# Kernel optimization log

Measured on AMD Instinct MI355X. Metric: run time of the kernel, lower is better.

The kernel has to match this reference:

```python
import jax, jax.numpy as jnp
import numpy as np

HEADS = 8
POINTS = 4
EPS = 1e-5


def _layernorm(x, w, b):
    m = jnp.mean(x, axis=-1, keepdims=True)
    v = jnp.var(x, axis=-1, keepdims=True)
    return (x - m) / jnp.sqrt(v + EPS) * w + b


def _msdeform_attn(x, ref, value, H, W, Wv, bv, Woff, boff, Wa, ba, Wout, bout):
    # x: (N, Lq, C) queries; value: (N, H*W, C); ref: (N, Lq, 1, 2) in [0,1]
    N, Lq, C = x.shape
    hd = C // HEADS
    # value projection, split heads -> (N, heads, HW, hd)
    v = (value @ Wv + bv).reshape(N, H * W, HEADS, hd).transpose(0, 2, 1, 3)
    # per-query learned offsets and attention weights
    off = (x @ Woff + boff).reshape(N, Lq, HEADS, POINTS, 2)
    attw = jax.nn.softmax((x @ Wa + ba).reshape(N, Lq, HEADS, POINTS), axis=-1)
    offset_normalizer = jnp.array([W, H], dtype=x.dtype)
    # sampling locations in normalized [0,1] coords: (N, Lq, heads, points, 2)
    loc = ref[:, :, None, :, :] + off / offset_normalizer
    # grid_sample bilinear, align_corners=False, zeros padding: pixel = loc*size - 0.5
    gx = loc[..., 0] * W - 0.5
    gy = loc[..., 1] * H - 0.5
    x0 = jnp.floor(gx)
    y0 = jnp.floor(gy)
    wx = gx - x0
    wy = gy - y0
    x0i = x0.astype(jnp.int32)
    y0i = y0.astype(jnp.int32)

    def gather(xi, yi):  # (N,Lq,heads,points) int -> (N,heads,Lq,points,hd), zero outside
        valid = ((xi >= 0) & (xi < W) & (yi >= 0) & (yi < H))
        idx = (jnp.clip(yi, 0, H - 1) * W + jnp.clip(xi, 0, W - 1)).transpose(0, 2, 1, 3)
        g = jnp.take_along_axis(v, idx.reshape(N, HEADS, Lq * POINTS)[..., None], axis=2)
        return g.reshape(N, HEADS, Lq, POINTS, hd) * valid.transpose(0, 2, 1, 3)[..., None].astype(v.dtype)

    def cw(w_):  # corner weight to (N,heads,Lq,points,1)
        return w_.transpose(0, 2, 1, 3)[..., None]

    samp = (gather(x0i, y0i) * cw((1 - wx) * (1 - wy))
            + gather(x0i + 1, y0i) * cw(wx * (1 - wy))
            + gather(x0i, y0i + 1) * cw((1 - wx) * wy)
            + gather(x0i + 1, y0i + 1) * cw(wx * wy))
    out = jnp.einsum('nhlpd,nlhp->nlhd', samp, attw).reshape(N, Lq, C)
    return out @ Wout + bout


def setup_inputs() -> dict:
    key = jax.random.key(0)
    ks = jax.random.split(key, 12)
    N, Lq, C, H, W = 4, 6400, 256, 80, 80
    hid = 4 * C
    hp2 = HEADS * POINTS * 2
    hp = HEADS * POINTS

    def w(k, shape, s=0.02):
        return jax.random.normal(k, shape, dtype=jnp.float32) * s

    return {
        'x': jax.random.normal(ks[0], (N, Lq, C), dtype=jnp.float32),
        'ref': jax.random.uniform(ks[1], (N, Lq, 1, 2), dtype=jnp.float32),
        'value': jax.random.normal(ks[2], (N, Lq, C), dtype=jnp.float32),
        'H': H, 'W': W,
        'ln1_w': jnp.ones((C,), jnp.float32), 'ln1_b': jnp.zeros((C,), jnp.float32),
        'ln2_w': jnp.ones((C,), jnp.float32), 'ln2_b': jnp.zeros((C,), jnp.float32),
        'Wv': w(ks[3], (C, C)), 'bv': jnp.zeros((C,), jnp.float32),
        'Woff': w(ks[4], (C, hp2), 0.01), 'boff': w(ks[5], (hp2,), 0.5),
        'Wa': w(ks[6], (C, hp)), 'ba': jnp.zeros((hp,), jnp.float32),
        'Wout': w(ks[7], (C, C)), 'bout': jnp.zeros((C,), jnp.float32),
        'W1': w(ks[8], (C, hid)), 'b1': jnp.zeros((hid,), jnp.float32),
        'W2': w(ks[9], (hid, C)), 'b2': jnp.zeros((C,), jnp.float32),
    }


def reference(x, ref, value, H, W, ln1_w, ln1_b, ln2_w, ln2_b, Wv, bv, Woff, boff, Wa, ba, Wout, bout, W1, b1, W2, b2):
    # x = x + attn(norm1(x), ref, value); LayerScale/DropPath are identity (init_values=None, drop_path=0)
    a = _msdeform_attn(_layernorm(x, ln1_w, ln1_b), ref, value, H, W, Wv, bv, Woff, boff, Wa, ba, Wout, bout)
    x = x + a
    # x = x + mlp(norm2(x))
    h = _layernorm(x, ln2_w, ln2_b)
    h = jax.nn.gelu(h @ W1 + b1, approximate=False)
    return x + (h @ W2 + b2)
```

## Files before the change

kernel.cpp:

```cpp
#include <hip/hip_runtime.h>

#define NB    4
#define LQ    6400
#define CC    256
#define HH    80
#define WW    80
#define HWSZ  (HH*WW)
#define RTOT  (NB*LQ)
#define HID   1024

typedef __attribute__((ext_vector_type(8))) short bf16x8;
typedef __attribute__((ext_vector_type(4))) float f32x4;

__device__ __forceinline__ float bf2f(unsigned short u) {
    unsigned int i = ((unsigned int)u) << 16;
    float f; __builtin_memcpy(&f, &i, 4); return f;
}
__device__ __forceinline__ unsigned short f2bf(float f) {
    unsigned int i; __builtin_memcpy(&i, &f, 4);
    unsigned int r = i + 0x7fffu + ((i >> 16) & 1u);
    return (unsigned short)(r >> 16);
}

__global__ void cvt_k(const float* __restrict__ in, unsigned short* __restrict__ out, int n4) {
    int i = blockIdx.x * 256 + threadIdx.x;
    if (i < n4) {
        float4 u = ((const float4*)in)[i];
        ushort4 o;
        o.x = f2bf(u.x); o.y = f2bf(u.y); o.z = f2bf(u.z); o.w = f2bf(u.w);
        ((ushort4*)out)[i] = o;
    }
}

__global__ void prep_k(const float* __restrict__ Wv,   const float* __restrict__ Wout,
                       const float* __restrict__ W1,   const float* __restrict__ W2,
                       const float* __restrict__ Woff, const float* __restrict__ Wa,
                       const float* __restrict__ boff, const float* __restrict__ ba,
                       unsigned short* __restrict__ wtv,  unsigned short* __restrict__ woutS,
                       unsigned short* __restrict__ w1s,  unsigned short* __restrict__ w2s,
                       unsigned short* __restrict__ woas, float* __restrict__ b_oa) {
    int idx = blockIdx.x * 256 + threadIdx.x;
    if (idx < 65536) {
        int n = idx >> 8, k = idx & 255;
        wtv[idx] = f2bf(Wv[(size_t)k * 256 + n]);
        return;
    }
    idx -= 65536;
    if (idx < 32768) {
        int n = idx & 1023, kq = idx >> 10;
        int kb = (kq >> 2) * 32 + (kq & 3) * 8;
        unsigned short* d = w1s + (size_t)idx * 8;
        #pragma unroll
        for (int j = 0; j < 8; ++j) d[j] = f2bf(W1[(size_t)(kb + j) * 1024 + n]);
        return;
    }
    idx -= 32768;
    if (idx < 32768) {
        int n = idx & 255, kq = idx >> 8;
        int kb = (kq >> 2) * 32 + (kq & 3) * 8;
        unsigned short* d = w2s + (size_t)idx * 8;
        #pragma unroll
        for (int j = 0; j < 8; ++j) d[j] = f2bf(W2[(size_t)(kb + j) * 256 + n]);
        return;
    }
    idx -= 32768;
    if (idx < 8192) {
        int n = idx & 255, kq = idx >> 8;
        int kb = (kq >> 2) * 32 + (kq & 3) * 8;
        unsigned short* d = woutS + (size_t)idx * 8;
        #pragma unroll
        for (int j = 0; j < 8; ++j) d[j] = f2bf(Wout[(size_t)(kb + j) * 256 + n]);
        return;
    }
    idx -= 8192;
    if (idx < 4096) {
        int n = idx & 127, kq = idx >> 7;
        int kb = (kq >> 2) * 32 + (kq & 3) * 8;
        unsigned short* d = woas + (size_t)idx * 8;
        #pragma unroll
        for (int j = 0; j < 8; ++j) {
            float v = 0.f;
            if (n < 64)      v = Woff[(size_t)(kb + j) * 64 + n];
            else if (n < 96) v = Wa[(size_t)(kb + j) * 32 + (n - 64)];
            d[j] = f2bf(v);
        }
        return;
    }
    idx -= 4096;
    if (idx < 96) b_oa[idx] = idx < 64 ? boff[idx] : ba[idx - 64];
}

__device__ __forceinline__ void ln_stage(const float* __restrict__ xbase,
                                         const float* __restrict__ lw,
                                         const float* __restrict__ lb,
                                         unsigned short* hblob, int t) {
    int r = t >> 3, sub = t & 7;
    const float* xr = xbase + (size_t)r * CC;
    float4 xv[4][2];
    float s = 0.f, s2 = 0.f;
    #pragma unroll
    for (int jj = 0; jj < 4; ++jj) {
        #pragma unroll
        for (int u = 0; u < 2; ++u) {
            float4 v = *(const float4*)(xr + sub * 8 + jj * 64 + u * 4);
            xv[jj][u] = v;
            s  += v.x + v.y + v.z + v.w;
            s2 += v.x*v.x + v.y*v.y + v.z*v.z + v.w*v.w;
        }
    }
    #pragma unroll
    for (int m = 1; m < 8; m <<= 1) {
        s  += __shfl_xor(s,  m);
        s2 += __shfl_xor(s2, m);
    }
    float mean = s * (1.0f / CC);
    float var  = s2 * (1.0f / CC) - mean * mean;
    float rstd = rsqrtf(fmaxf(var, 0.0f) + 1e-5f);
    #pragma unroll
    for (int jj = 0; jj < 4; ++jj) {
        int c0 = sub * 8 + jj * 64;
        float4 w0 = *(const float4*)(lw + c0);
        float4 w1 = *(const float4*)(lw + c0 + 4);
        float4 bb0 = *(const float4*)(lb + c0);
        float4 bb1 = *(const float4*)(lb + c0 + 4);
        bf16x8 o;
        o[0] = (short)f2bf((xv[jj][0].x - mean) * rstd * w0.x + bb0.x);
        o[1] = (short)f2bf((xv[jj][0].y - mean) * rstd * w0.y + bb0.y);
        o[2] = (short)f2bf((xv[jj][0].z - mean) * rstd * w0.z + bb0.z);
        o[3] = (short)f2bf((xv[jj][0].w - mean) * rstd * w0.w + bb0.w);
        o[4] = (short)f2bf((xv[jj][1].x - mean) * rstd * w1.x + bb1.x);
        o[5] = (short)f2bf((xv[jj][1].y - mean) * rstd * w1.y + bb1.y);
        o[6] = (short)f2bf((xv[jj][1].z - mean) * rstd * w1.z + bb1.z);
        o[7] = (short)f2bf((xv[jj][1].w - mean) * rstd * w1.w + bb1.w);
        int kq = sub + jj * 8;
        *(bf16x8*)((char*)hblob + kq * 1040 + r * 16) = o;
    }
}

template<int EPI, bool OF32>
__global__ __launch_bounds__(256) void gemm_t(const unsigned short* __restrict__ A,
                                              const unsigned short* __restrict__ Bt,
                                              const float* __restrict__ bias,
                                              const float* __restrict__ res,
                                              void* __restrict__ Cout_,
                                              int M, int Nv, int K) {
    __shared__ unsigned short Als[64 * 32];
    __shared__ unsigned short Bls[128 * 32];
    int lane = threadIdx.x & 63;
    int wave = threadIdx.x >> 6;
    int quad = lane >> 4;
    int l16  = lane & 15;
    int m0 = blockIdx.x * 64;
    int n0 = blockIdx.y * 128;
    int wm = (wave & 1) * 32;
    int wn = (wave >> 1) * 64;

    f32x4 acc[2][4];
    #pragma unroll
    for (int i = 0; i < 2; ++i)
        #pragma unroll
        for (int j = 0; j < 4; ++j)
            acc[i][j] = (f32x4){0.f, 0.f, 0.f, 0.f};

    int srow = lane >> 2;
    int scol = (lane & 3) * 8;
    const unsigned short* Ag = A  + (size_t)(m0 + wave * 16 + srow) * K + scol;
    const unsigned short* Bg = Bt + (size_t)(n0 + wave * 32 + srow) * K + scol;
    unsigned short* Alp = &Als[wave * 512];
    unsigned short* Blp = &Bls[wave * 1024];

    for (int k0 = 0; k0 < K; k0 += 32) {
        __syncthreads();
        __builtin_amdgcn_global_load_lds(
            (const __attribute__((address_space(1))) void*)(Ag + k0),
            (__attribute__((address_space(3))) void*)Alp, 16, 0, 0);
        #pragma unroll
        for (int t = 0; t < 2; ++t) {
            __builtin_amdgcn_global_load_lds(
                (const __attribute__((address_space(1))) void*)(Bg + (size_t)t * 16 * K + k0),
                (__attribute__((address_space(3))) void*)(Blp + t * 512), 16, 0, 0);
        }
        __builtin_amdgcn_s_waitcnt(0);
        __syncthreads();

        bf16x8 af[2], bfr[4];
        #pragma unroll
        for (int i = 0; i < 2; ++i)
            af[i] = *(const bf16x8*)&Als[(wm + i * 16 + l16) * 32 + quad * 8];
        #pragma unroll
        for (int j = 0; j < 4; ++j)
            bfr[j] = *(const bf16x8*)&Bls[(wn + j * 16 + l16) * 32 + quad * 8];
        #pragma unroll
        for (int i = 0; i < 2; ++i)
            #pragma unroll
            for (int j = 0; j < 4; ++j)
                acc[i][j] = __builtin_amdgcn_mfma_f32_16x16x32_bf16(af[i], bfr[j], acc[i][j], 0, 0, 0);
    }

    #pragma unroll
    for (int j = 0; j < 4; ++j) {
        int cbase = n0 + wn + j * 16;
        if (cbase >= Nv) continue;
        int col = cbase + l16;
        float bv = bias[col];
        #pragma unroll
        for (int i = 0; i < 2; ++i) {
            #pragma unroll
            for (int r = 0; r < 4; ++r) {
                int row = m0 + wm + i * 16 + quad * 4 + r;
                float val = acc[i][j][r] + bv;
                if (EPI == 2) val += res[(size_t)row * Nv + col];
                if (OF32) ((float*)Cout_)[(size_t)row * Nv + col] = val;
                else      ((unsigned short*)Cout_)[(size_t)row * Nv + col] = f2bf(val);
            }
        }
    }
}

__global__ __launch_bounds__(512) void lnoa_k(
        const float* __restrict__ x, const float* __restrict__ lw, const float* __restrict__ lb,
        const unsigned short* __restrict__ woas, const float* __restrict__ b_oa,
        unsigned short* __restrict__ oa) {
    __shared__ char lds_raw[33280];
    unsigned short* hblob = (unsigned short*)lds_raw;
    int t = threadIdx.x;
    int lane = t & 63, wave = t >> 6;
    int quad = lane >> 4, l16 = lane & 15;
    int row0 = blockIdx.x * 64;

    ln_stage(x + (size_t)row0 * CC, lw, lb, hblob, t);
    __syncthreads();

    if (wave < 6) {
        f32x4 acc[4];
        #pragma unroll
        for (int qt = 0; qt < 4; ++qt) acc[qt] = (f32x4){0.f, 0.f, 0.f, 0.f};
        #pragma unroll
        for (int kb = 0; kb < 8; ++kb) {
            bf16x8 a1 = *(const bf16x8*)(woas + ((size_t)(kb * 4 + quad) * 128 + wave * 16 + l16) * 8);
            #pragma unroll
            for (int qt = 0; qt < 4; ++qt) {
                bf16x8 bf = *(const bf16x8*)((char*)hblob + (kb * 4 + quad) * 1040 + (qt * 16 + l16) * 16);
                acc[qt] = __builtin_amdgcn_mfma_f32_16x16x32_bf16(a1, bf, acc[qt], 0, 0, 0);
            }
        }
        int n0 = wave * 16 + quad * 4;
        float4 bb = *(const float4*)(b_oa + n0);
        const float* bp = (const float*)&bb;
        #pragma unroll
        for (int qt = 0; qt < 4; ++qt) {
            unsigned long long pk = 0;
            #pragma unroll
            for (int r = 0; r < 4; ++r)
                pk |= ((unsigned long long)f2bf(acc[qt][r] + bp[r])) << (16 * r);
            *(unsigned long long*)(oa + (size_t)(row0 + qt * 16 + l16) * 96 + n0) = pk;
        }
    }
}

__global__ __launch_bounds__(512) void samwout_k(
        const unsigned short* __restrict__ v,
        const float* __restrict__ ref,
        const unsigned short* __restrict__ oa,
        const unsigned short* __restrict__ woutS,
        const float* __restrict__ bout,
        const float* __restrict__ x,
        float* __restrict__ x2) {
    __shared__ char lds_raw[57856];
    unsigned short* hblob = (unsigned short*)lds_raw;
    short4* sidx = (short4*)(lds_raw + 33280);
    float4* sw   = (float4*)(lds_raw + 41472);
    float* trans = (float*)lds_raw;

    int t = threadIdx.x;
    int lane = t & 63, wave = t >> 6;
    int quad = lane >> 4, l16 = lane & 15;
    int row0 = blockIdx.x * 64;
    int nb = blockIdx.x / (LQ / 64);

    for (int half = 0; half < 2; ++half) {
        int rbase = half * 32;
        #pragma unroll
        for (int s = 0; s < 2; ++s) {
            int e = t + s * 512;
            int q = e >> 5, sub = e & 31, h = sub >> 2, p = sub & 3;
            int row = row0 + rbase + q;
            float refx = ref[row * 2 + 0];
            float refy = ref[row * 2 + 1];
            const unsigned short* oar = oa + (size_t)row * 96;
            float ox = bf2f(oar[(h * 4 + p) * 2 + 0]);
            float oy = bf2f(oar[(h * 4 + p) * 2 + 1]);
            float l  = bf2f(oar[64 + h * 4 + p]);
            float m = fmaxf(l, __shfl_xor(l, 1));
            m = fmaxf(m, __shfl_xor(m, 2));
            float ee = __expf(l - m);
            float ss = ee + __shfl_xor(ee, 1);
            ss = ss + __shfl_xor(ss, 2);
            float wp = ee / ss;

            float gx = (refx + ox * (1.0f / WW)) * WW - 0.5f;
            float gy = (refy + oy * (1.0f / HH)) * HH - 0.5f;
            float fx = floorf(gx), fy = floorf(gy);
            float wx = gx - fx, wy = gy - fy;
            int x0 = (int)fx, y0 = (int)fy;
            int x1 = x0 + 1, y1 = y0 + 1;
            bool vx0 = (unsigned)x0 < WW, vx1 = (unsigned)x1 < WW;
            bool vy0 = (unsigned)y0 < HH, vy1 = (unsigned)y1 < HH;
            float w00 = (vx0 && vy0) ? wp * (1.f - wx) * (1.f - wy) : 0.f;
            float w10 = (vx1 && vy0) ? wp * wx * (1.f - wy)         : 0.f;
            float w01 = (vx0 && vy1) ? wp * (1.f - wx) * wy         : 0.f;
            float w11 = (vx1 && vy1) ? wp * wx * wy                 : 0.f;
            int cx0 = min(max(x0, 0), WW - 1), cx1 = min(max(x1, 0), WW - 1);
            int cy0 = min(max(y0, 0), HH - 1), cy1 = min(max(y1, 0), HH - 1);
            sidx[e] = (short4){(short)(cy0 * WW + cx0), (short)(cy0 * WW + cx1),
                               (short)(cy1 * WW + cx0), (short)(cy1 * WW + cx1)};
            sw[e]   = (float4){w00, w10, w01, w11};
        }
        __syncthreads();
        #pragma unroll
        for (int s = 0; s < 2; ++s) {
            int c = t + s * 512;
            int q = c >> 5, sub = c & 31, h = sub >> 2, cg = sub & 3;
            const unsigned short* base = v + (size_t)nb * HWSZ * CC + h * 32 + cg * 8;
            float acc[8];
            #pragma unroll
            for (int j = 0; j < 8; ++j) acc[j] = 0.f;
            #pragma unroll
            for (int p = 0; p < 4; ++p) {
                int e = q * 32 + h * 4 + p;
                short4 I = sidx[e];
                float4 Wt = sw[e];
                const short* Ip = (const short*)&I;
                const float* Wp = (const float*)&Wt;
                #pragma unroll
                for (int cn = 0; cn < 4; ++cn) {
                    bf16x8 u = *(const bf16x8*)(base + (size_t)(unsigned short)Ip[cn] * CC);
                    float wgt = Wp[cn];
                    #pragma unroll
                    for (int j = 0; j < 8; ++j)
                        acc[j] += wgt * bf2f((unsigned short)u[j]);
                }
            }
            bf16x8 o;
            #pragma unroll
            for (int j = 0; j < 8; ++j) o[j] = (short)f2bf(acc[j]);
            *(bf16x8*)((char*)hblob + sub * 1040 + (rbase + q) * 16) = o;
        }
        __syncthreads();
    }

    f32x4 acc2[2][4];
    #pragma unroll
    for (int a = 0; a < 2; ++a)
        #pragma unroll
        for (int b = 0; b < 4; ++b)
            acc2[a][b] = (f32x4){0.f, 0.f, 0.f, 0.f};
    #pragma unroll
    for (int kb = 0; kb < 8; ++kb) {
        bf16x8 a2[2], bf[4];
        #pragma unroll
        for (int ct = 0; ct < 2; ++ct)
            a2[ct] = *(const bf16x8*)(woutS + ((size_t)(kb * 4 + quad) * 256 + wave * 32 + ct * 16 + l16) * 8);
        #pragma unroll
        for (int qt = 0; qt < 4; ++qt)
            bf[qt] = *(const bf16x8*)((char*)hblob + (kb * 4 + quad) * 1040 + (qt * 16 + l16) * 16);
        #pragma unroll
        for (int ct = 0; ct < 2; ++ct)
            #pragma unroll
            for (int qt = 0; qt < 4; ++qt)
                acc2[ct][qt] = __builtin_amdgcn_mfma_f32_16x16x32_bf16(a2[ct], bf[qt], acc2[ct][qt], 0, 0, 0);
    }

    for (int p = 0; p < 2; ++p) {
        __syncthreads();
        #pragma unroll
        for (int qi = 0; qi < 2; ++qi) {
            int qt = p * 2 + qi;
            int qlocal = qt * 16 + l16 - p * 32;
            #pragma unroll
            for (int ct = 0; ct < 2; ++ct) {
                int c4 = wave * 8 + ct * 4 + quad;
                *(f32x4*)(trans + qlocal * 260 + c4 * 4) = acc2[ct][qt];
            }
        }
        __syncthreads();
        int rr = t >> 4;
        int c4b = t & 15;
        int row = row0 + p * 32 + rr;
        #pragma unroll
        for (int i = 0; i < 4; ++i) {
            int c4 = i * 16 + c4b;
            f32x4 vv = *(const f32x4*)(trans + rr * 260 + c4 * 4);
            int c = c4 * 4;
            float4 xv = *(const float4*)(x + (size_t)row * CC + c);
            float4 bb = *(const float4*)(bout + c);
            float4 o;
            o.x = vv[0] + xv.x + bb.x;
            o.y = vv[1] + xv.y + bb.y;
            o.z = vv[2] + xv.z + bb.z;
            o.w = vv[3] + xv.w + bb.w;
            *(float4*)(x2 + (size_t)row * CC + c) = o;
        }
    }
}

__global__ __launch_bounds__(512) void mlp_k(
        const float* __restrict__ x2,
        const float* __restrict__ lw,
        const float* __restrict__ lb,
        const unsigned short* __restrict__ w1s,
        const float* __restrict__ b1,
        const unsigned short* __restrict__ w2s,
        const float* __restrict__ b2,
        float* __restrict__ out) {
    __shared__ char lds_raw[66560];
    unsigned short* hblob = (unsigned short*)lds_raw;
    unsigned short* h1b0  = (unsigned short*)(lds_raw + 33280);
    unsigned short* h1b1  = (unsigned short*)(lds_raw + 49920);
    float* trans = (float*)lds_raw;

    int t = threadIdx.x;
    int lane = t & 63, wave = t >> 6;
    int quad = lane >> 4, l16 = lane & 15;
    int row0 = blockIdx.x * 64;

    ln_stage(x2 + (size_t)row0 * CC, lw, lb, hblob, t);
    __syncthreads();

    f32x4 acc2[2][4];
    #pragma unroll
    for (int a = 0; a < 2; ++a)
        #pragma unroll
        for (int b = 0; b < 4; ++b)
            acc2[a][b] = (f32x4){0.f, 0.f, 0.f, 0.f};

    auto s1 = [&](int hc, unsigned short* dst) {
        f32x4 a[4];
        #pragma unroll
        for (int qt = 0; qt < 4; ++qt) a[qt] = (f32x4){0.f, 0.f, 0.f, 0.f};
        #pragma unroll
        for (int kb = 0; kb < 8; ++kb) {
            bf16x8 a1 = *(const bf16x8*)(w1s + ((size_t)(kb * 4 + quad) * 1024 + hc * 128 + wave * 16 + l16) * 8);
            #pragma unroll
            for (int qt = 0; qt < 4; ++qt) {
                bf16x8 bf = *(const bf16x8*)((char*)hblob + (kb * 4 + quad) * 1040 + (qt * 16 + l16) * 16);
                a[qt] = __builtin_amdgcn_mfma_f32_16x16x32_bf16(a1, bf, a[qt], 0, 0, 0);
            }
        }
        int hl = wave * 16 + quad * 4;
        float4 bb = *(const float4*)(b1 + hc * 128 + hl);
        const float* bp = (const float*)&bb;
        #pragma unroll
        for (int qt = 0; qt < 4; ++qt) {
            unsigned long long pk = 0;
            #pragma unroll
            for (int r = 0; r < 4; ++r) {
                float val = a[qt][r] + bp[r];
                val = 0.5f * val * (1.0f + erff(val * 0.70710678118654752f));
                pk |= ((unsigned long long)f2bf(val)) << (16 * r);
            }
            *(unsigned long long*)((char*)dst + (hl >> 3) * 1040 + (qt * 16 + l16) * 16 + (hl & 7) * 2) = pk;
        }
    };

    auto s2 = [&](int hc, const unsigned short* src) {
        #pragma unroll
        for (int k2 = 0; k2 < 4; ++k2) {
            bf16x8 a2[2], bf[4];
            #pragma unroll
            for (int ct = 0; ct < 2; ++ct)
                a2[ct] = *(const bf16x8*)(w2s + ((size_t)((hc * 4 + k2) * 4 + quad) * 256 + wave * 32 + ct * 16 + l16) * 8);
            #pragma unroll
            for (int qt = 0; qt < 4; ++qt)
                bf[qt] = *(const bf16x8*)((const char*)src + (k2 * 4 + quad) * 1040 + (qt * 16 + l16) * 16);
            #pragma unroll
            for (int ct = 0; ct < 2; ++ct)
                #pragma unroll
                for (int qt = 0; qt < 4; ++qt)
                    acc2[ct][qt] = __builtin_amdgcn_mfma_f32_16x16x32_bf16(a2[ct], bf[qt], acc2[ct][qt], 0, 0, 0);
        }
    };

    s1(0, h1b0);
    for (int hc = 0; hc < 8; ++hc) {
        __syncthreads();
        const unsigned short* cur = (hc & 1) ? h1b1 : h1b0;
        unsigned short*       nxt = (hc & 1) ? h1b0 : h1b1;
        s2(hc, cur);
        if (hc < 7) s1(hc + 1, nxt);
    }
    __syncthreads();

    #pragma unroll
    for (int qt = 0; qt < 4; ++qt) {
        int qrow = qt * 16 + l16;
        #pragma unroll
        for (int ct = 0; ct < 2; ++ct) {
            int c4 = wave * 8 + ct * 4 + quad;
            *(f32x4*)(trans + qrow * 260 + c4 * 4) = acc2[ct][qt];
        }
    }
    __syncthreads();
    {
        int rr = t >> 3;
        int c4b = t & 7;
        int row = row0 + rr;
        #pragma unroll
        for (int i = 0; i < 8; ++i) {
            int c4 = i * 8 + c4b;
            f32x4 v = *(const f32x4*)(trans + rr * 260 + c4 * 4);
            int c = c4 * 4;
            float4 xv = *(const float4*)(x2 + (size_t)row * CC + c);
            float4 bb = *(const float4*)(b2 + c);
            float4 o;
            o.x = v[0] + xv.x + bb.x;
            o.y = v[1] + xv.y + bb.y;
            o.z = v[2] + xv.z + bb.z;
            o.w = v[3] + xv.w + bb.w;
            *(float4*)(out + (size_t)row * CC + c) = o;
        }
    }
}

extern "C" void kernel_launch(void* const* d_in, const int* in_sizes, int n_in,
                              void* d_out, int out_size, void* d_ws, size_t ws_size,
                              hipStream_t stream) {
    const float* x     = (const float*)d_in[0];
    const float* ref   = (const float*)d_in[1];
    const float* value = (const float*)d_in[2];
    const float* ln1w  = (const float*)d_in[5];
    const float* ln1b  = (const float*)d_in[6];
    const float* ln2w  = (const float*)d_in[7];
    const float* ln2b  = (const float*)d_in[8];
    const float* Wv    = (const float*)d_in[9];
    const float* bv    = (const float*)d_in[10];
    const float* Woff  = (const float*)d_in[11];
    const float* boff  = (const float*)d_in[12];
    const float* Wa    = (const float*)d_in[13];
    const float* ba    = (const float*)d_in[14];
    const float* Wout  = (const float*)d_in[15];
    const float* bout  = (const float*)d_in[16];
    const float* W1    = (const float*)d_in[17];
    const float* b1    = (const float*)d_in[18];
    const float* W2    = (const float*)d_in[19];
    const float* b2    = (const float*)d_in[20];

    char* ws = (char*)d_ws;
    unsigned short* wtv_b  = (unsigned short*)(ws + 0);
    unsigned short* wouts_b= (unsigned short*)(ws + 131072);
    unsigned short* w1s_b  = (unsigned short*)(ws + 262144);
    unsigned short* w2s_b  = (unsigned short*)(ws + 786432);
    unsigned short* woas_b = (unsigned short*)(ws + 1310720);
    float*          b_oa   = (float*)         (ws + 1376256);
    float*          x2_f   = (float*)         (ws + 1376768);
    unsigned short* val_b  = (unsigned short*)(ws + 27591168);
    unsigned short* v_b    = (unsigned short*)(ws + 40698368);
    unsigned short* oa_b   = (unsigned short*)(ws + 53805568);

    prep_k<<<561, 256, 0, stream>>>(Wv, Wout, W1, W2, Woff, Wa, boff, ba,
                                    wtv_b, wouts_b, w1s_b, w2s_b, woas_b, b_oa);
    cvt_k<<<(RTOT*CC/4 + 255) / 256, 256, 0, stream>>>(value, val_b, RTOT*CC/4);
    gemm_t<0, false><<<dim3(RTOT/64, 2), 256, 0, stream>>>(val_b, wtv_b, bv, nullptr, v_b, RTOT, 256, 256);
    lnoa_k<<<RTOT/64, 512, 0, stream>>>(x, ln1w, ln1b, woas_b, b_oa, oa_b);
    samwout_k<<<RTOT/64, 512, 0, stream>>>(v_b, ref, oa_b, wouts_b, bout, x, x2_f);
    mlp_k<<<RTOT/64, 512, 0, stream>>>(x2_f, ln2w, ln2b, w1s_b, b1, w2s_b, b2, (float*)d_out);
}
```

Baseline: 224.6 us.

## Fuse weight prep with value cast, merge value GEMM into LN/offset kernel, split MLP waves

Merges the weight-prep and value-conversion launches into one kernel. It replaces the standalone value-projection GEMM with a branch of a combined kernel that also runs the LayerNorm plus offset/attention projection, so fewer kernels launch. The MLP kernel now assigns four waves as producers computing the GELU hidden chunks and four as consumers doing the second GEMM, overlapping the two stages via double buffering. This cuts launch count and serial stalls inside the MLP, but doubles per-wave accumulator registers in the consumer path and raises LDS use in the merged kernel, which may lower occupancy.

```diff
diff --git a/kernel.cpp b/kernel.cpp
--- a/kernel.cpp
+++ b/kernel.cpp
@@ -22,30 +22,33 @@
     return (unsigned short)(r >> 16);
 }
 
-__global__ void cvt_k(const float* __restrict__ in, unsigned short* __restrict__ out, int n4) {
-    int i = blockIdx.x * 256 + threadIdx.x;
-    if (i < n4) {
-        float4 u = ((const float4*)in)[i];
+__global__ void prepcvt_k(const float* __restrict__ value, unsigned short* __restrict__ val_b,
+                          const float* __restrict__ Wv,   const float* __restrict__ Wout,
+                          const float* __restrict__ W1,   const float* __restrict__ W2,
+                          const float* __restrict__ Woff, const float* __restrict__ Wa,
+                          const float* __restrict__ boff, const float* __restrict__ ba,
+                          unsigned short* __restrict__ wvS,  unsigned short* __restrict__ woutS,
+                          unsigned short* __restrict__ w1s,  unsigned short* __restrict__ w2s,
+                          unsigned short* __restrict__ woas, float* __restrict__ b_oa) {
+    int b = blockIdx.x;
+    if (b < 6400) {
+        int i = b * 256 + threadIdx.x;
+        float4 u = ((const float4*)value)[i];
         ushort4 o;
         o.x = f2bf(u.x); o.y = f2bf(u.y); o.z = f2bf(u.z); o.w = f2bf(u.w);
-        ((ushort4*)out)[i] = o;
-    }
-}
-
-__global__ void prep_k(const float* __restrict__ Wv,   const float* __restrict__ Wout,
-                       const float* __restrict__ W1,   const float* __restrict__ W2,
-                       const float* __restrict__ Woff, const float* __restrict__ Wa,
-                       const float* __restrict__ boff, const float* __restrict__ ba,
-                       unsigned short* __restrict__ wtv,  unsigned short* __restrict__ woutS,
-                       unsigned short* __restrict__ w1s,  unsigned short* __restrict__ w2s,
-                       unsigned short* __restrict__ woas, float* __restrict__ b_oa) {
-    int idx = blockIdx.x * 256 + threadIdx.x;
-    if (idx < 65536) {
-        int n = idx >> 8, k = idx & 255;
-        wtv[idx] = f2bf(Wv[(size_t)k * 256 + n]);
+        ((ushort4*)val_b)[i] = o;
         return;
     }
-    idx -= 65536;
+    int idx = (b - 6400) * 256 + threadIdx.x;
+    if (idx < 8192) {
+        int n = idx & 255, kq = idx >> 8;
+        int kb = (kq >> 2) * 32 + (kq & 3) * 8;
+        unsigned short* d = wvS + (size_t)idx * 8;
+        #pragma unroll
+        for (int j = 0; j < 8; ++j) d[j] = f2bf(Wv[(size_t)(kb + j) * 256 + n]);
+        return;
+    }
+    idx -= 8192;
     if (idx < 32768) {
         int n = idx & 1023, kq = idx >> 10;
         int kb = (kq >> 2) * 32 + (kq & 3) * 8;
@@ -137,123 +140,108 @@
     }
 }
 
-template<int EPI, bool OF32>
-__global__ __launch_bounds__(256) void gemm_t(const unsigned short* __restrict__ A,
-                                              const unsigned short* __restrict__ Bt,
-                                              const float* __restrict__ bias,
-                                              const float* __restrict__ res,
-                                              void* __restrict__ Cout_,
-                                              int M, int Nv, int K) {
-    __shared__ unsigned short Als[64 * 32];
-    __shared__ unsigned short Bls[128 * 32];
-    int lane = threadIdx.x & 63;
-    int wave = threadIdx.x >> 6;
-    int quad = lane >> 4;
-    int l16  = lane & 15;
-    int m0 = blockIdx.x * 64;
-    int n0 = blockIdx.y * 128;
-    int wm = (wave & 1) * 32;
-    int wn = (wave >> 1) * 64;
-
-    f32x4 acc[2][4];
-    #pragma unroll
-    for (int i = 0; i < 2; ++i)
-        #pragma unroll
-        for (int j = 0; j < 4; ++j)
-            acc[i][j] = (f32x4){0.f, 0.f, 0.f, 0.f};
-
-    int srow = lane >> 2;
-    int scol = (lane & 3) * 8;
-    const unsigned short* Ag = A  + (size_t)(m0 + wave * 16 + srow) * K + scol;
-    const unsigned short* Bg = Bt + (size_t)(n0 + wave * 32 + srow) * K + scol;
-    unsigned short* Alp = &Als[wave * 512];
-    unsigned short* Blp = &Bls[wave * 1024];
-
-    for (int k0 = 0; k0 < K; k0 += 32) {
-        __syncthreads();
-        __builtin_amdgcn_global_load_lds(
-            (const __attribute__((address_space(1))) void*)(Ag + k0),
-            (__attribute__((address_space(3))) void*)Alp, 16, 0, 0);
-        #pragma unroll
-        for (int t = 0; t < 2; ++t) {
-            __builtin_amdgcn_global_load_lds(
-                (const __attribute__((address_space(1))) void*)(Bg + (size_t)t * 16 * K + k0),
-                (__attribute__((address_space(3))) void*)(Blp + t * 512), 16, 0, 0);
-        }
-        __builtin_amdgcn_s_waitcnt(0);
-        __syncthreads();
-
-        bf16x8 af[2], bfr[4];
-        #pragma unroll
-        for (int i = 0; i < 2; ++i)
-            af[i] = *(const bf16x8*)&Als[(wm + i * 16 + l16) * 32 + quad * 8];
-        #pragma unroll
-        for (int j = 0; j < 4; ++j)
-            bfr[j] = *(const bf16x8*)&Bls[(wn + j * 16 + l16) * 32 + quad * 8];
-        #pragma unroll
-        for (int i = 0; i < 2; ++i)
-            #pragma unroll
-            for (int j = 0; j < 4; ++j)
-                acc[i][j] = __builtin_amdgcn_mfma_f32_16x16x32_bf16(af[i], bfr[j], acc[i][j], 0, 0, 0);
-    }
-
-    #pragma unroll
-    for (int j = 0; j < 4; ++j) {
-        int cbase = n0 + wn + j * 16;
-        if (cbase >= Nv) continue;
-        int col = cbase + l16;
-        float bv = bias[col];
-        #pragma unroll
-        for (int i = 0; i < 2; ++i) {
-            #pragma unroll
-            for (int r = 0; r < 4; ++r) {
-                int row = m0 + wm + i * 16 + quad * 4 + r;
-                float val = acc[i][j][r] + bv;
-                if (EPI == 2) val += res[(size_t)row * Nv + col];
-                if (OF32) ((float*)Cout_)[(size_t)row * Nv + col] = val;
-                else      ((unsigned short*)Cout_)[(size_t)row * Nv + col] = f2bf(val);
-            }
-        }
-    }
-}
-
-__global__ __launch_bounds__(512) void lnoa_k(
+__global__ __launch_bounds__(512) void pl_k(
+        const unsigned short* __restrict__ val_b, const unsigned short* __restrict__ wvS,
+        const float* __restrict__ bv,
         const float* __restrict__ x, const float* __restrict__ lw, const float* __restrict__ lb,
         const unsigned short* __restrict__ woas, const float* __restrict__ b_oa,
-        unsigned short* __restrict__ oa) {
-    __shared__ char lds_raw[33280];
+        unsigned short* __restrict__ v_b, unsigned short* __restrict__ oa) {
+    __shared__ char lds_raw[66560];
     unsigned short* hblob = (unsigned short*)lds_raw;
+    float* trans = (float*)lds_raw;
+
+    int b = blockIdx.x;
     int t = threadIdx.x;
     int lane = t & 63, wave = t >> 6;
     int quad = lane >> 4, l16 = lane & 15;
-    int row0 = blockIdx.x * 64;
-
-    ln_stage(x + (size_t)row0 * CC, lw, lb, hblob, t);
-    __syncthreads();
-
-    if (wave < 6) {
-        f32x4 acc[4];
-        #pragma unroll
-        for (int qt = 0; qt < 4; ++qt) acc[qt] = (f32x4){0.f, 0.f, 0.f, 0.f};
+
+    if (b < 400) {
+        int row0 = b * 64;
+        {
+            int kq = t & 31, rb = t >> 5;
+            #pragma unroll
+            for (int i = 0; i < 4; ++i) {
+                int r = i * 16 + rb;
+                bf16x8 u = *(const bf16x8*)(val_b + (size_t)(row0 + r) * CC + kq * 8);
+                *(bf16x8*)((char*)hblob + kq * 1040 + r * 16) = u;
+            }
+        }
+        __syncthreads();
+        f32x4 acc[2][4];
+        #pragma unroll
+        for (int a = 0; a < 2; ++a)
+            #pragma unroll
+            for (int q = 0; q < 4; ++q)
+                acc[a][q] = (f32x4){0.f, 0.f, 0.f, 0.f};
         #pragma unroll
         for (int kb = 0; kb < 8; ++kb) {
-            bf16x8 a1 = *(const bf16x8*)(woas + ((size_t)(kb * 4 + quad) * 128 + wave * 16 + l16) * 8);
+            bf16x8 a2[2], bf[4];
+            #pragma unroll
+            for (int ct = 0; ct < 2; ++ct)
+                a2[ct] = *(const bf16x8*)(wvS + ((size_t)(kb * 4 + quad) * 256 + wave * 32 + ct * 16 + l16) * 8);
+            #pragma unroll
+            for (int qt = 0; qt < 4; ++qt)
+                bf[qt] = *(const bf16x8*)((char*)hblob + (kb * 4 + quad) * 1040 + (qt * 16 + l16) * 16);
+            #pragma unroll
+            for (int ct = 0; ct < 2; ++ct)
+                #pragma unroll
+                for (int qt = 0; qt < 4; ++qt)
+                    acc[ct][qt] = __builtin_amdgcn_mfma_f32_16x16x32_bf16(a2[ct], bf[qt], acc[ct][qt], 0, 0, 0);
+        }
+        __syncthreads();
+        #pragma unroll
+        for (int qt = 0; qt < 4; ++qt) {
+            int qrow = qt * 16 + l16;
+            #pragma unroll
+            for (int ct = 0; ct < 2; ++ct) {
+                int c4 = wave * 8 + ct * 4 + quad;
+                *(f32x4*)(trans + qrow * 260 + c4 * 4) = acc[ct][qt];
+            }
+        }
+        __syncthreads();
+        {
+            int rr = t >> 3, c4b = t & 7;
+            #pragma unroll
+            for (int i = 0; i < 8; ++i) {
+                int c4 = i * 8 + c4b;
+                f32x4 vv = *(const f32x4*)(trans + rr * 260 + c4 * 4);
+                float4 bb = *(const float4*)(bv + c4 * 4);
+                ushort4 o;
+                o.x = f2bf(vv[0] + bb.x);
+                o.y = f2bf(vv[1] + bb.y);
+                o.z = f2bf(vv[2] + bb.z);
+                o.w = f2bf(vv[3] + bb.w);
+                *(ushort4*)(v_b + (size_t)(row0 + rr) * CC + c4 * 4) = o;
+            }
+        }
+    } else {
+        int row0 = (b - 400) * 64;
+        ln_stage(x + (size_t)row0 * CC, lw, lb, hblob, t);
+        __syncthreads();
+        if (wave < 6) {
+            f32x4 acc[4];
+            #pragma unroll
+            for (int qt = 0; qt < 4; ++qt) acc[qt] = (f32x4){0.f, 0.f, 0.f, 0.f};
+            #pragma unroll
+            for (int kb = 0; kb < 8; ++kb) {
+                bf16x8 a1 = *(const bf16x8*)(woas + ((size_t)(kb * 4 + quad) * 128 + wave * 16 + l16) * 8);
+                #pragma unroll
+                for (int qt = 0; qt < 4; ++qt) {
+                    bf16x8 bf = *(const bf16x8*)((char*)hblob + (kb * 4 + quad) * 1040 + (qt * 16 + l16) * 16);
+                    acc[qt] = __builtin_amdgcn_mfma_f32_16x16x32_bf16(a1, bf, acc[qt], 0, 0, 0);
+                }
+            }
+            int n0 = wave * 16 + quad * 4;
+            float4 bb = *(const float4*)(b_oa + n0);
+            const float* bp = (const float*)&bb;
             #pragma unroll
             for (int qt = 0; qt < 4; ++qt) {
-                bf16x8 bf = *(const bf16x8*)((char*)hblob + (kb * 4 + quad) * 1040 + (qt * 16 + l16) * 16);
-                acc[qt] = __builtin_amdgcn_mfma_f32_16x16x32_bf16(a1, bf, acc[qt], 0, 0, 0);
-            }
-        }
-        int n0 = wave * 16 + quad * 4;
-        float4 bb = *(const float4*)(b_oa + n0);
-        const float* bp = (const float*)&bb;
-        #pragma unroll
-        for (int qt = 0; qt < 4; ++qt) {
-            unsigned long long pk = 0;
-            #pragma unroll
-            for (int r = 0; r < 4; ++r)
-                pk |= ((unsigned long long)f2bf(acc[qt][r] + bp[r])) << (16 * r);
-            *(unsigned long long*)(oa + (size_t)(row0 + qt * 16 + l16) * 96 + n0) = pk;
+                unsigned long long pk = 0;
+                #pragma unroll
+                for (int r = 0; r < 4; ++r)
+                    pk |= ((unsigned long long)f2bf(acc[qt][r] + bp[r])) << (16 * r);
+                *(unsigned long long*)(oa + (size_t)(row0 + qt * 16 + l16) * 96 + n0) = pk;
+            }
         }
     }
 }
@@ -423,87 +411,101 @@
     int lane = t & 63, wave = t >> 6;
     int quad = lane >> 4, l16 = lane & 15;
     int row0 = blockIdx.x * 64;
+    bool producer = wave < 4;
+    int pw = wave & 3;
 
     ln_stage(x2 + (size_t)row0 * CC, lw, lb, hblob, t);
-    __syncthreads();
-
-    f32x4 acc2[2][4];
+
+    f32x4 acc2[4][4];
     #pragma unroll
-    for (int a = 0; a < 2; ++a)
+    for (int a = 0; a < 4; ++a)
         #pragma unroll
         for (int b = 0; b < 4; ++b)
             acc2[a][b] = (f32x4){0.f, 0.f, 0.f, 0.f};
 
     auto s1 = [&](int hc, unsigned short* dst) {
-        f32x4 a[4];
-        #pragma unroll
-        for (int qt = 0; qt < 4; ++qt) a[qt] = (f32x4){0.f, 0.f, 0.f, 0.f};
+        f32x4 a[2][4];
+        #pragma unroll
+        for (int ht = 0; ht < 2; ++ht)
+            #pragma unroll
+            for (int qt = 0; qt < 4; ++qt) a[ht][qt] = (f32x4){0.f, 0.f, 0.f, 0.f};
         #pragma unroll
         for (int kb = 0; kb < 8; ++kb) {
-            bf16x8 a1 = *(const bf16x8*)(w1s + ((size_t)(kb * 4 + quad) * 1024 + hc * 128 + wave * 16 + l16) * 8);
+            bf16x8 a1[2], bf[4];
+            #pragma unroll
+            for (int ht = 0; ht < 2; ++ht)
+                a1[ht] = *(const bf16x8*)(w1s + ((size_t)(kb * 4 + quad) * 1024 + hc * 128 + pw * 32 + ht * 16 + l16) * 8);
+            #pragma unroll
+            for (int qt = 0; qt < 4; ++qt)
+                bf[qt] = *(const bf16x8*)((char*)hblob + (kb * 4 + quad) * 1040 + (qt * 16 + l16) * 16);
+            #pragma unroll
+            for (int ht = 0; ht < 2; ++ht)
+                #pragma unroll
+                for (int qt = 0; qt < 4; ++qt)
+                    a[ht][qt] = __builtin_amdgcn_mfma_f32_16x16x32_bf16(a1[ht], bf[qt], a[ht][qt], 0, 0, 0);
+        }
+        #pragma unroll
+        for (int ht = 0; ht < 2; ++ht) {
+            int hl = pw * 32 + ht * 16 + quad * 4;
+            float4 bb = *(const float4*)(b1 + hc * 128 + hl);
+            const float* bp = (const float*)&bb;
             #pragma unroll
             for (int qt = 0; qt < 4; ++qt) {
-                bf16x8 bf = *(const bf16x8*)((char*)hblob + (kb * 4 + quad) * 1040 + (qt * 16 + l16) * 16);
-                a[qt] = __builtin_amdgcn_mfma_f32_16x16x32_bf16(a1, bf, a[qt], 0, 0, 0);
-            }
-        }
-        int hl = wave * 16 + quad * 4;
-        float4 bb = *(const float4*)(b1 + hc * 128 + hl);
-        const float* bp = (const float*)&bb;
-        #pragma unroll
-        for (int qt = 0; qt < 4; ++qt) {
-            unsigned long long pk = 0;
-            #pragma unroll
-            for (int r = 0; r < 4; ++r) {
-                float val = a[qt][r] + bp[r];
-                val = 0.5f * val * (1.0f + erff(val * 0.70710678118654752f));
-                pk |= ((unsigned long long)f2bf(val)) << (16 * r);
-            }
-            *(unsigned long long*)((char*)dst + (hl >> 3) * 1040 + (qt * 16 + l16) * 16 + (hl & 7) * 2) = pk;
+                unsigned long long pk = 0;
+                #pragma unroll
+                for (int r = 0; r < 4; ++r) {
+                    float val = a[ht][qt][r] + bp[r];
+                    val = 0.5f * val * (1.0f + erff(val * 0.70710678118654752f));
+                    pk |= ((unsigned long long)f2bf(val)) << (16 * r);
+                }
+                *(unsigned long long*)((char*)dst + (hl >> 3) * 1040 + (qt * 16 + l16) * 16 + (hl & 7) * 2) = pk;
+            }
         }
     };
 
     auto s2 = [&](int hc, const unsigned short* src) {
         #pragma unroll
         for (int k2 = 0; k2 < 4; ++k2) {
-            bf16x8 a2[2], bf[4];
-            #pragma unroll
-            for (int ct = 0; ct < 2; ++ct)
-                a2[ct] = *(const bf16x8*)(w2s + ((size_t)((hc * 4 + k2) * 4 + quad) * 256 + wave * 32 + ct * 16 + l16) * 8);
+            bf16x8 a2[4], bf[4];
+            #pragma unroll
+            for (int ct = 0; ct < 4; ++ct)
+                a2[ct] = *(const bf16x8*)(w2s + ((size_t)((hc * 4 + k2) * 4 + quad) * 256 + pw * 64 + ct * 16 + l16) * 8);
             #pragma unroll
             for (int qt = 0; qt < 4; ++qt)
                 bf[qt] = *(const bf16x8*)((const char*)src + (k2 * 4 + quad) * 1040 + (qt * 16 + l16) * 16);
             #pragma unroll
-            for (int ct = 0; ct < 2; ++ct)
+            for (int ct = 0; ct < 4; ++ct)
                 #pragma unroll
                 for (int qt = 0; qt < 4; ++qt)
                     acc2[ct][qt] = __builtin_amdgcn_mfma_f32_16x16x32_bf16(a2[ct], bf[qt], acc2[ct][qt], 0, 0, 0);
         }
     };
 
-    s1(0, h1b0);
+    __syncthreads();
+    if (producer) s1(0, h1b0);
+    __syncthreads();
     for (int hc = 0; hc < 8; ++hc) {
-        __syncthreads();
         const unsigned short* cur = (hc & 1) ? h1b1 : h1b0;
         unsigned short*       nxt = (hc & 1) ? h1b0 : h1b1;
-        s2(hc, cur);
-        if (hc < 7) s1(hc + 1, nxt);
-    }
-    __syncthreads();
-
-    #pragma unroll
-    for (int qt = 0; qt < 4; ++qt) {
-        int qrow = qt * 16 + l16;
-        #pragma unroll
-        for (int ct = 0; ct < 2; ++ct) {
-            int c4 = wave * 8 + ct * 4 + quad;
-            *(f32x4*)(trans + qrow * 260 + c4 * 4) = acc2[ct][qt];
+        if (producer) { if (hc < 7) s1(hc + 1, nxt); }
+        else          s2(hc, cur);
+        __syncthreads();
+    }
+
+    if (!producer) {
+        #pragma unroll
+        for (int qt = 0; qt < 4; ++qt) {
+            int qrow = qt * 16 + l16;
+            #pragma unroll
+            for (int ct = 0; ct < 4; ++ct) {
+                int c4 = pw * 16 + ct * 4 + quad;
+                *(f32x4*)(trans + qrow * 260 + c4 * 4) = acc2[ct][qt];
+            }
         }
     }
     __syncthreads();
     {
-        int rr = t >> 3;
-        int c4b = t & 7;
+        int rr = t >> 3, c4b = t & 7;
         int row = row0 + rr;
         #pragma unroll
         for (int i = 0; i < 8; ++i) {
@@ -546,7 +548,7 @@
     const float* b2    = (const float*)d_in[20];
 
     char* ws = (char*)d_ws;
-    unsigned short* wtv_b  = (unsigned short*)(ws + 0);
+    unsigned short* wvs_b  = (unsigned short*)(ws + 0);
     unsigned short* wouts_b= (unsigned short*)(ws + 131072);
     unsigned short* w1s_b  = (unsigned short*)(ws + 262144);
     unsigned short* w2s_b  = (unsigned short*)(ws + 786432);
@@ -557,11 +559,9 @@
     unsigned short* v_b    = (unsigned short*)(ws + 40698368);
     unsigned short* oa_b   = (unsigned short*)(ws + 53805568);
 
-    prep_k<<<561, 256, 0, stream>>>(Wv, Wout, W1, W2, Woff, Wa, boff, ba,
-                                    wtv_b, wouts_b, w1s_b, w2s_b, woas_b, b_oa);
-    cvt_k<<<(RTOT*CC/4 + 255) / 256, 256, 0, stream>>>(value, val_b, RTOT*CC/4);
-    gemm_t<0, false><<<dim3(RTOT/64, 2), 256, 0, stream>>>(val_b, wtv_b, bv, nullptr, v_b, RTOT, 256, 256);
-    lnoa_k<<<RTOT/64, 512, 0, stream>>>(x, ln1w, ln1b, woas_b, b_oa, oa_b);
+    prepcvt_k<<<6737, 256, 0, stream>>>(value, val_b, Wv, Wout, W1, W2, Woff, Wa, boff, ba,
+                                        wvs_b, wouts_b, w1s_b, w2s_b, woas_b, b_oa);
+    pl_k<<<800, 512, 0, stream>>>(val_b, wvs_b, bv, x, ln1w, ln1b, woas_b, b_oa, v_b, oa_b);
     samwout_k<<<RTOT/64, 512, 0, stream>>>(v_b, ref, oa_b, wouts_b, bout, x, x2_f);
     mlp_k<<<RTOT/64, 512, 0, stream>>>(x2_f, ln2w, ln2b, w1s_b, b1, w2s_b, b2, (float*)d_out);
 }
```

Measured after the change: 262.8 us. 17.0% more time.
